# Kernel tuning notes

Measured on AMD Instinct MI355X. Metric: run time of the kernel, lower is better.

## Reference

```python
import jax, jax.numpy as jnp
import numpy as np

NC, NPR, E, B = 200000, 100000, 500000, 200000
DIN, HID, HEADS = 16, 256, 8
D = HID // HEADS
NCOLOR, NSIZE, NGROUP = 1000, 30, 50


def setup_inputs() -> dict:
    key = jax.random.key(0)
    ks = jax.random.split(key, 24)
    g = lambda i, shape, s=0.05: jax.random.normal(ks[i], shape, jnp.float32) * s
    return dict(
        customer_x=g(0, (NC, DIN), 1.0),
        product_x=g(1, (NPR, DIN), 1.0),
        proj_cust_W=g(2, (DIN, HID)), proj_cust_b=jnp.zeros((HID,), jnp.float32),
        proj_prod_W=g(3, (DIN, HID)), proj_prod_b=jnp.zeros((HID,), jnp.float32),
        att_src_r=g(4, (HEADS, D)), att_dst_r=g(5, (HEADS, D)),
        att_src_rb=g(6, (HEADS, D)), att_dst_rb=g(7, (HEADS, D)),
        q_sem=g(8, (HID,)), k_lin_W=g(9, (HID, HID)), k_lin_b=jnp.zeros((HID,), jnp.float32),
        color_emb=g(10, (NCOLOR, 8), 1.0),
        size_emb=g(11, (NSIZE, 4), 1.0),
        group_emb=g(12, (NGROUP, 4), 1.0),
        fc1_W=g(13, (HID * 2 + 16, 128)), fc1_b=jnp.zeros((128,), jnp.float32),
        fc2_W=g(14, (128, 32)), fc2_b=jnp.zeros((32,), jnp.float32),
        fc3_W=g(15, (32, 1)), fc3_b=jnp.zeros((1,), jnp.float32),
        bn1_gamma=jnp.ones((128,), jnp.float32), bn1_beta=jnp.zeros((128,), jnp.float32),
        bn2_gamma=jnp.ones((32,), jnp.float32), bn2_beta=jnp.zeros((32,), jnp.float32),
        edge_src=jax.random.randint(ks[16], (E,), 0, NC),
        edge_dst=jax.random.randint(ks[17], (E,), 0, NPR),
        label_src=jax.random.randint(ks[18], (B,), 0, NC),
        label_dst=jax.random.randint(ks[19], (B,), 0, NPR),
        size_idx=jax.random.randint(ks[20], (B,), 0, NSIZE),
        color_idx=jax.random.randint(ks[21], (B,), 0, NCOLOR),
        group_idx=jax.random.randint(ks[22], (B,), 0, NGROUP),
    )


def _edge_softmax(logits, dst, n):
    # destination-grouped softmax over edges; logits: [E,H]
    m = jax.ops.segment_max(logits, dst, num_segments=n)
    m = jnp.where(jnp.isfinite(m), m, 0.0)
    e = jnp.exp(logits - m[dst])
    s = jax.ops.segment_sum(e, dst, num_segments=n)
    return e / (s[dst] + 1e-16)


def _han_relation(h_src, h_dst, a_src, a_dst, src, dst, n_dst):
    # h_*: [N,H,D]; a_*: [H,D]
    logits = (h_src * a_src).sum(-1)[src] + (h_dst * a_dst).sum(-1)[dst]  # [E,H]
    logits = jax.nn.leaky_relu(logits, 0.2)
    alpha = _edge_softmax(logits, dst, n_dst)
    msg = alpha[:, :, None] * h_src[src]  # [E,H,D]
    out = jax.ops.segment_sum(msg, dst, num_segments=n_dst)
    return jax.nn.relu(out.reshape(n_dst, -1))  # [N_dst, H*D]


def _group(outs, q, kW, kb):
    # semantic attention over metapaths (PyG HANConv group)
    stk = jnp.stack(outs)  # [M,N,F]
    score = (q * jnp.tanh(stk @ kW + kb).mean(1)).sum(-1)  # [M]
    attn = jax.nn.softmax(score)
    return jnp.einsum('m,mnf->nf', attn, stk)


def _bn(x, gamma, beta):
    mu = x.mean(0)
    var = x.var(0)
    return (x - mu) * jax.lax.rsqrt(var + 1e-5) * gamma + beta


def reference(customer_x, product_x, proj_cust_W, proj_cust_b, proj_prod_W, proj_prod_b,
              att_src_r, att_dst_r, att_src_rb, att_dst_rb, q_sem, k_lin_W, k_lin_b,
              color_emb, size_emb, group_emb, fc1_W, fc1_b, fc2_W, fc2_b, fc3_W, fc3_b,
              bn1_gamma, bn1_beta, bn2_gamma, bn2_beta,
              edge_src, edge_dst, label_src, label_dst, size_idx, color_idx, group_idx):
    h_c = (customer_x @ proj_cust_W + proj_cust_b).reshape(-1, HEADS, D)
    h_p = (product_x @ proj_prod_W + proj_prod_b).reshape(-1, HEADS, D)
    # relation customer -returns-> product
    out_p = _han_relation(h_c, h_p, att_src_r, att_dst_r, edge_src, edge_dst, NPR)
    # relation product -returned_by-> customer (reversed edges)
    out_c = _han_relation(h_p, h_c, att_src_rb, att_dst_rb, edge_dst, edge_src, NC)
    cust = _group([out_c], q_sem, k_lin_W, k_lin_b)  # [NC, 256]
    prod = _group([out_p], q_sem, k_lin_W, k_lin_b)  # [NPR, 256]
    feat = jnp.concatenate([cust[label_src], prod[label_dst],
                            size_emb[size_idx], color_emb[color_idx], group_emb[group_idx]], axis=-1)
    x = jax.nn.relu(feat @ fc1_W + fc1_b)
    x = _bn(x, bn1_gamma, bn1_beta)
    x = jax.nn.relu(x @ fc2_W + fc2_b)
    x = _bn(x, bn2_gamma, bn2_beta)
    return x @ fc3_W + fc3_b
```

## Files before the change

kernel.cpp:

```cpp
#include <hip/hip_runtime.h>

#define NCC 200000
#define NPRR 100000
#define NEE 500000
#define NBB 200000

typedef __attribute__((ext_vector_type(8))) short bf16x8;
typedef __attribute__((ext_vector_type(16))) float f32x16;

__device__ __forceinline__ float b2f(unsigned short u){ return __uint_as_float(((unsigned)u)<<16); }
__device__ __forceinline__ unsigned short f2b(float f){
  unsigned x = __float_as_uint(f);
  return (unsigned short)((x + 0x7fffu + ((x>>16)&1u)) >> 16);
}

__global__ __launch_bounds__(256) void wa_prep2(
    const float* __restrict__ Wc, const float* __restrict__ bc,
    const float* __restrict__ attAc, const float* __restrict__ attBc,
    const float* __restrict__ Wp, const float* __restrict__ bp,
    const float* __restrict__ attAp, const float* __restrict__ attBp,
    float* __restrict__ WAc, float* __restrict__ WAp)
{
  int tid = threadIdx.x;
  for (int task = tid; task < 4*17*8; task += 256) {
    int grp = task / 136, rem = task % 136;
    int k = rem >> 3, h = rem & 7;
    const float* att = (grp==0)?attAc:(grp==1)?attBc:(grp==2)?attAp:attBp;
    const float* W   = (grp<2)?Wc:Wp;
    const float* bias= (grp<2)?bc:bp;
    const float* row = (k < 16) ? (W + k*256) : bias;
    float acc = 0.f;
    for (int d = 0; d < 32; d++) acc = fmaf(row[h*32+d], att[h*32+d], acc);
    if (grp<2) WAc[(grp&1)*136 + rem] = acc;
    else       WAp[(grp&1)*136 + rem] = acc;
  }
}

__global__ __launch_bounds__(256) void prep_proj(
    const float* __restrict__ Wc, const float* __restrict__ Wp,
    const float* __restrict__ WAc, const float* __restrict__ WAp,
    unsigned short* __restrict__ WtC, unsigned short* __restrict__ WtP,
    unsigned short* __restrict__ WAtC, unsigned short* __restrict__ WAtP)
{
  int idx = blockIdx.x*256 + threadIdx.x;
  if (idx < 4096){ int n=idx>>4, k=idx&15; WtC[idx]=f2b(Wc[k*256+n]); }
  else if (idx < 8192){ int t=idx-4096; int n=t>>4, k=t&15; WtP[t]=f2b(Wp[k*256+n]); }
  else if (idx < 8704){ int t=idx-8192; int n=t>>4, k=t&15;
    WAtC[t] = (n<16)? f2b(WAc[(n>>3)*136 + k*8 + (n&7)]) : (unsigned short)0; }
  else if (idx < 9216){ int t=idx-8704; int n=t>>4, k=t&15;
    WAtP[t] = (n<16)? f2b(WAp[(n>>3)*136 + k*8 + (n&7)]) : (unsigned short)0; }
}

__global__ __launch_bounds__(256) void prep_fc1(const float* __restrict__ fc1W,
    const float* __restrict__ fc1b,
    const float* __restrict__ size_emb, const float* __restrict__ color_emb,
    const float* __restrict__ group_emb,
    unsigned short* __restrict__ BtC, unsigned short* __restrict__ BtP,
    float* __restrict__ Ts, float* __restrict__ Tc, float* __restrict__ Tg)
{
  int idx = blockIdx.x*256 + threadIdx.x;
  if (idx < 32768){
    int n = idx>>8, k = idx&255;
    BtC[idx] = f2b(fc1W[k*128 + n]);
  } else if (idx < 65536){
    int t = idx - 32768;
    int n = t>>8, k = t&255;
    BtP[t] = f2b(fc1W[(256+k)*128 + n]);
  } else if (idx < 65536 + 30*128){
    int t = idx - 65536;
    int s = t>>7, j = t&127;
    float a = fc1b[j];
    #pragma unroll
    for (int c=0;c<4;c++) a = fmaf(size_emb[s*4+c], fc1W[(512+c)*128+j], a);
    Ts[t] = a;
  } else if (idx < 65536 + 30*128 + 1000*128){
    int t = idx - 65536 - 30*128;
    int col = t>>7, j = t&127;
    float a = 0.f;
    #pragma unroll
    for (int c=0;c<8;c++) a = fmaf(color_emb[col*8+c], fc1W[(516+c)*128+j], a);
    Tc[t] = a;
  } else if (idx < 65536 + 30*128 + 1000*128 + 50*128){
    int t = idx - 65536 - 30*128 - 1000*128;
    int g = t>>7, j = t&127;
    float a = 0.f;
    #pragma unroll
    for (int c=0;c<4;c++) a = fmaf(group_emb[g*4+c], fc1W[(524+c)*128+j], a);
    Tg[t] = a;
  }
}

__global__ __launch_bounds__(256) void proj_mfma(const float* __restrict__ X,
    const unsigned short* __restrict__ Wt, const unsigned short* __restrict__ WAt,
    const float* __restrict__ WA,
    unsigned short* __restrict__ H, float* __restrict__ sA, float* __restrict__ sB,
    int N, int nt)
{
  __shared__ unsigned short wt[4608];
  __shared__ float biasS[16];
  int tid = threadIdx.x;
  for (int i=tid; i<512; i+=256) ((uint4*)wt)[i] = ((const uint4*)Wt)[i];
  for (int i=tid; i<64;  i+=256) ((uint4*)(wt+4096))[i] = ((const uint4*)WAt)[i];
  if (tid < 16) biasS[tid] = WA[(tid>>3)*136 + 128 + (tid&7)];
  __syncthreads();
  int wv = tid>>6, lane = tid&63, m = lane&31, hi = lane>>5;
  for (int t = blockIdx.x; t < nt; t += gridDim.x){
    int node = t*32 + m;
    bf16x8 a;
    {
      const float4* xr = (const float4*)(X + (long long)node*16 + hi*8);
      float4 f0 = xr[0], f1 = xr[1];
      unsigned short av[8] = {f2b(f0.x),f2b(f0.y),f2b(f0.z),f2b(f0.w),
                              f2b(f1.x),f2b(f1.y),f2b(f1.z),f2b(f1.w)};
      a = *(bf16x8*)av;
    }
    #pragma unroll
    for (int s=0;s<2;s++){
      int c0 = wv*64 + s*32;
      bf16x8 b = *(const bf16x8*)(wt + (c0+m)*16 + hi*8);
      f32x16 acc;
      #pragma unroll
      for (int i=0;i<16;i++) acc[i]=0.f;
      acc = __builtin_amdgcn_mfma_f32_32x32x16_bf16(a, b, acc, 0, 0, 0);
      #pragma unroll
      for (int reg=0; reg<16; reg++){
        int row = (reg&3) + 8*(reg>>2) + 4*hi;
        H[(long long)(t*32+row)*256 + c0 + m] = f2b(acc[reg]);
      }
    }
    if (wv == 0){
      bf16x8 b = *(const bf16x8*)(wt + 4096 + m*16 + hi*8);
      f32x16 acc;
      #pragma unroll
      for (int i=0;i<16;i++) acc[i]=0.f;
      acc = __builtin_amdgcn_mfma_f32_32x32x16_bf16(a, b, acc, 0, 0, 0);
      if (m < 16){
        float bias = biasS[m];
        float* dst = (m < 8) ? sA : sB;
        int h = m & 7;
        #pragma unroll
        for (int reg=0; reg<16; reg++){
          int row = (reg&3) + 8*(reg>>2) + 4*hi;
          dst[(long long)(t*32+row)*8 + h] = acc[reg] + bias;
        }
      }
    }
  }
}

__global__ __launch_bounds__(256) void hist2(const int* __restrict__ src, const int* __restrict__ dst,
    int* __restrict__ cnt_c, int* __restrict__ cnt_p, int E)
{
  int e = blockIdx.x*256 + threadIdx.x;
  if (e >= E) return;
  atomicAdd(&cnt_p[dst[e]], 1);
  atomicAdd(&cnt_c[src[e]], 1);
}

__global__ __launch_bounds__(256) void scan_phase1(const int* __restrict__ cnt, int* __restrict__ bsum, int N)
{
  __shared__ int red[256];
  int tid = threadIdx.x;
  int base = blockIdx.x*1024 + tid*4;
  int s = 0;
  #pragma unroll
  for (int k=0;k<4;k++){ int i=base+k; if (i<N) s += cnt[i]; }
  red[tid] = s;
  __syncthreads();
  for (int off=128; off>0; off>>=1){ if (tid<off) red[tid]+=red[tid+off]; __syncthreads(); }
  if (tid==0) bsum[blockIdx.x] = red[0];
}

__global__ __launch_bounds__(256) void scan_phase2(int* __restrict__ bsum, int B,
    int* __restrict__ rowptr, int N)
{
  __shared__ int ts[256];
  int tid = threadIdx.x;
  int v = (tid<B) ? bsum[tid] : 0;
  ts[tid] = v;
  __syncthreads();
  for (int off=1; off<256; off<<=1){
    int t = (tid>=off) ? ts[tid-off] : 0;
    __syncthreads();
    ts[tid] += t;
    __syncthreads();
  }
  if (tid < B) bsum[tid] = ts[tid] - v;
  if (tid == B-1) rowptr[N] = ts[tid];
}

__global__ __launch_bounds__(256) void scan_phase3(const int* __restrict__ cnt,
    const int* __restrict__ bsum, int* __restrict__ rowptr, int N)
{
  __shared__ int ts[256];
  int tid = threadIdx.x;
  int base = blockIdx.x*1024 + tid*4;
  int v[4]; int s = 0;
  #pragma unroll
  for (int k=0;k<4;k++){ int i=base+k; v[k] = (i<N) ? cnt[i] : 0; s += v[k]; }
  ts[tid] = s;
  __syncthreads();
  for (int off=1; off<256; off<<=1){
    int t = (tid>=off) ? ts[tid-off] : 0;
    __syncthreads();
    ts[tid] += t;
    __syncthreads();
  }
  int run = bsum[blockIdx.x] + ts[tid] - s;
  #pragma unroll
  for (int k=0;k<4;k++){ int i=base+k; if (i<N){ rowptr[i]=run; run += v[k]; } }
}

__global__ __launch_bounds__(256) void place2(const int* __restrict__ src, const int* __restrict__ dst,
    const int* __restrict__ rp_r, const int* __restrict__ rp_rb,
    int* __restrict__ cnt_p, int* __restrict__ cnt_c,
    int* __restrict__ si_r, int* __restrict__ si_rb, int E)
{
  int e = blockIdx.x*256 + threadIdx.x;
  if (e >= E) return;
  int s = src[e], d = dst[e];
  si_r [rp_r [d] + atomicAdd(&cnt_p[d], 1)] = s;
  si_rb[rp_rb[s] + atomicAdd(&cnt_c[s], 1)] = d;
}

__global__ __launch_bounds__(256) void agg_gemm(
    const int* __restrict__ rowptr, const int* __restrict__ srcidx,
    const float* __restrict__ sSrc, const float* __restrict__ sDst,
    const unsigned short* __restrict__ H, const unsigned short* __restrict__ Bt,
    unsigned short* __restrict__ Y)
{
  __shared__ unsigned short feat[32*264];
  int tid = threadIdx.x;
  int wv = tid>>6, lane = tid&63;
  int g = lane>>4, ln = lane&15, h = ln>>1;
  long long base = (long long)blockIdx.x*32;
  #pragma unroll
  for (int t=0;t<2;t++){
    int r = wv*8 + t*4 + g;
    long long n = base + r;
    int e  = rowptr[n], e1 = rowptr[n+1];
    float sdh = sDst[n*8 + h];
    float acc[16];
    #pragma unroll
    for (int c=0;c<16;c++) acc[c]=0.f;
    float den = 0.f;
    while (__any(e < e1)){
      if (e < e1){
        int s0 = srcidx[e];
        bool has2 = (e+1 < e1);
        int s1 = has2 ? srcidx[e+1] : s0;
        const uint4* p0 = (const uint4*)&H[(long long)s0*256 + ln*16];
        const uint4* p1 = (const uint4*)&H[(long long)s1*256 + ln*16];
        uint4 uA0 = p0[0], uA1 = p0[1];
        uint4 uB0 = p1[0], uB1 = p1[1];
        float l0 = sSrc[(long long)s0*8 + h] + sdh;
        float l1 = sSrc[(long long)s1*8 + h] + sdh;
        float w0 = __expf(l0 > 0.f ? l0 : 0.2f*l0);
        float w1 = has2 ? __expf(l1 > 0.f ? l1 : 0.2f*l1) : 0.f;
        den += w0 + w1;
        unsigned ua[8] = {uA0.x,uA0.y,uA0.z,uA0.w, uA1.x,uA1.y,uA1.z,uA1.w};
        unsigned ub[8] = {uB0.x,uB0.y,uB0.z,uB0.w, uB1.x,uB1.y,uB1.z,uB1.w};
        #pragma unroll
        for (int p=0;p<8;p++){
          acc[p*2]   = fmaf(w0, b2f((unsigned short)(ua[p]&0xffffu)), acc[p*2]);
          acc[p*2+1] = fmaf(w0, b2f((unsigned short)(ua[p]>>16)),     acc[p*2+1]);
          acc[p*2]   = fmaf(w1, b2f((unsigned short)(ub[p]&0xffffu)), acc[p*2]);
          acc[p*2+1] = fmaf(w1, b2f((unsigned short)(ub[p]>>16)),     acc[p*2+1]);
        }
        e += 2;
      }
    }
    float inv = 1.f/(den + 1e-16f);
    unsigned short ov[16];
    #pragma unroll
    for (int c=0;c<16;c++) ov[c] = f2b(fmaxf(acc[c]*inv, 0.f));
    *(uint4*)&feat[r*264 + ln*16]     = *(uint4*)&ov[0];
    *(uint4*)&feat[r*264 + ln*16 + 8] = *(uint4*)&ov[8];
  }
  __syncthreads();
  int m = lane&31, hi = lane>>5;
  f32x16 acc;
  #pragma unroll
  for (int i=0;i<16;i++) acc[i]=0.f;
  const unsigned short* ap  = feat + m*264 + hi*8;
  const unsigned short* btp = Bt + (wv*32 + m)*256 + hi*8;
  #pragma unroll 4
  for (int ks=0; ks<16; ks++){
    bf16x8 a = *(const bf16x8*)(ap + ks*16);
    bf16x8 b = *(const bf16x8*)(btp + ks*16);
    acc = __builtin_amdgcn_mfma_f32_32x32x16_bf16(a, b, acc, 0, 0, 0);
  }
  int col = wv*32 + m;
  #pragma unroll
  for (int reg=0; reg<16; reg++){
    int row = (reg&3) + 8*(reg>>2) + 4*hi;
    Y[(base+row)*128 + col] = f2b(acc[reg]);
  }
}

__global__ __launch_bounds__(256) void gather_fc1(
    const unsigned short* __restrict__ Yc, const unsigned short* __restrict__ Yp,
    const float* __restrict__ Ts, const float* __restrict__ Tc, const float* __restrict__ Tg,
    const int* __restrict__ lsrc, const int* __restrict__ ldst,
    const int* __restrict__ sidx, const int* __restrict__ cidx, const int* __restrict__ gidx,
    unsigned short* __restrict__ x1, float* __restrict__ bnsum, int ntiles)
{
  __shared__ float redS[16][128];
  __shared__ float redQ[16][128];
  int tid = threadIdx.x;
  int rl = tid>>4, g = tid&15;
  float sacc[8] = {0,0,0,0,0,0,0,0};
  float qacc[8] = {0,0,0,0,0,0,0,0};
  for (int t = blockIdx.x; t < ntiles; t += gridDim.x){
    long long row = (long long)t*16 + rl;
    int ls = lsrc[row], ld = ldst[row], si = sidx[row], ci = cidx[row], gi = gidx[row];
    uint4 uc = *(const uint4*)&Yc[(long long)ls*128 + g*8];
    uint4 up = *(const uint4*)&Yp[(long long)ld*128 + g*8];
    float4 t0 = *(const float4*)&Ts[si*128 + g*8];
    float4 t1 = *(const float4*)&Ts[si*128 + g*8 + 4];
    float4 c0 = *(const float4*)&Tc[ci*128 + g*8];
    float4 c1 = *(const float4*)&Tc[ci*128 + g*8 + 4];
    float4 g0 = *(const float4*)&Tg[gi*128 + g*8];
    float4 g1 = *(const float4*)&Tg[gi*128 + g*8 + 4];
    unsigned ucs[4] = {uc.x,uc.y,uc.z,uc.w};
    unsigned ups[4] = {up.x,up.y,up.z,up.w};
    float tb[8] = {t0.x+c0.x+g0.x, t0.y+c0.y+g0.y, t0.z+c0.z+g0.z, t0.w+c0.w+g0.w,
                   t1.x+c1.x+g1.x, t1.y+c1.y+g1.y, t1.z+c1.z+g1.z, t1.w+c1.w+g1.w};
    unsigned short ov[8];
    #pragma unroll
    for (int p=0;p<4;p++){
      float vl = b2f((unsigned short)(ucs[p]&0xffffu)) + b2f((unsigned short)(ups[p]&0xffffu)) + tb[p*2];
      float vh = b2f((unsigned short)(ucs[p]>>16))     + b2f((unsigned short)(ups[p]>>16))     + tb[p*2+1];
      vl = fmaxf(vl, 0.f); vh = fmaxf(vh, 0.f);
      ov[p*2] = f2b(vl); ov[p*2+1] = f2b(vh);
      sacc[p*2]   += vl; qacc[p*2]   += vl*vl;
      sacc[p*2+1] += vh; qacc[p*2+1] += vh*vh;
    }
    *(uint4*)&x1[row*128 + g*8] = *(uint4*)ov;
  }
  #pragma unroll
  for (int j=0;j<8;j++){ redS[rl][g*8+j]=sacc[j]; redQ[rl][g*8+j]=qacc[j]; }
  __syncthreads();
  if (tid < 128){
    float s=0.f, q=0.f;
    #pragma unroll
    for (int r=0;r<16;r++){ s += redS[r][tid]; q += redQ[r][tid]; }
    atomicAdd(&bnsum[tid], s);
    atomicAdd(&bnsum[128+tid], q);
  }
}

__global__ void bn1_fold(const float* __restrict__ bnsum,
    const float* __restrict__ gamma, const float* __restrict__ beta,
    const float* __restrict__ fc2W, const float* __restrict__ fc2b,
    unsigned short* __restrict__ Bt2, float* __restrict__ b2p, float invB)
{
  __shared__ float sc[128], sh[128];
  int tid = threadIdx.x;
  if (tid<128){
    float mu  = bnsum[tid]*invB;
    float var = bnsum[128+tid]*invB - mu*mu;
    float s = gamma[tid] * rsqrtf(var + 1e-5f);
    sc[tid]=s; sh[tid]= beta[tid] - mu*s;
  }
  __syncthreads();
  for (int idx=tid; idx<32*128; idx+=256){
    int n = idx>>7, k = idx&127;
    Bt2[idx] = f2b(sc[k]*fc2W[k*32+n]);
  }
  if (tid<32){
    float a = fc2b[tid];
    for (int k=0;k<128;k++) a = fmaf(sh[k], fc2W[k*32+tid], a);
    b2p[tid]=a;
  }
}

__global__ __launch_bounds__(256) void fc2_mfma(const unsigned short* __restrict__ x1,
    const unsigned short* __restrict__ Bt2, const float* __restrict__ b2p,
    unsigned short* __restrict__ x2, float* __restrict__ bnsum2, int M)
{
  __shared__ unsigned short xt[128*136];
  __shared__ unsigned short wt[32*136];
  __shared__ float redS[4][32];
  __shared__ float redQ[4][32];
  int tid = threadIdx.x;
  long long base = (long long)blockIdx.x*128;
  for (int idx=tid; idx<128*16; idx+=256){
    int r = idx>>4, c = idx&15;
    uint4 u = make_uint4(0,0,0,0);
    if (base + r < M) u = *(const uint4*)&x1[(base+r)*128 + c*8];
    *(uint4*)&xt[r*136 + c*8] = u;
  }
  for (int idx=tid; idx<32*16; idx+=256){
    int r = idx>>4, c = idx&15;
    *(uint4*)&wt[r*136 + c*8] = *(const uint4*)&Bt2[r*128 + c*8];
  }
  __syncthreads();
  int wv = tid>>6, lane = tid&63;
  int m = lane&31, hi = lane>>5;
  f32x16 acc;
  #pragma unroll
  for (int i=0;i<16;i++) acc[i]=0.f;
  const unsigned short* ap = xt + (wv*32 + m)*136 + hi*8;
  const unsigned short* bp = wt + m*136 + hi*8;
  #pragma unroll
  for (int ks=0; ks<8; ks++){
    bf16x8 a = *(const bf16x8*)(ap + ks*16);
    bf16x8 b = *(const bf16x8*)(bp + ks*16);
    acc = __builtin_amdgcn_mfma_f32_32x32x16_bf16(a, b, acc, 0, 0, 0);
  }
  int col = m;
  float bias = b2p[col];
  float s=0.f, q=0.f;
  #pragma unroll
  for (int reg=0; reg<16; reg++){
    int row = (reg&3) + 8*(reg>>2) + 4*hi;
    long long grow = base + wv*32 + row;
    float v = fmaxf(acc[reg] + bias, 0.f);
    if (grow < M) x2[grow*32 + col] = f2b(v);
    s += v; q += v*v;
  }
  if (base + 128 > M){
    s = 0.f; q = 0.f;
    #pragma unroll
    for (int reg=0; reg<16; reg++){
      int row = (reg&3) + 8*(reg>>2) + 4*hi;
      long long grow = base + wv*32 + row;
      float v = fmaxf(acc[reg] + bias, 0.f);
      if (grow < M){ s += v; q += v*v; }
    }
  }
  s += __shfl_xor(s, 32);
  q += __shfl_xor(q, 32);
  if (hi == 0){ redS[wv][col] = s; redQ[wv][col] = q; }
  __syncthreads();
  if (tid < 32){
    float a = redS[0][tid]+redS[1][tid]+redS[2][tid]+redS[3][tid];
    float b = redQ[0][tid]+redQ[1][tid]+redQ[2][tid]+redQ[3][tid];
    atomicAdd(&bnsum2[tid], a);
    atomicAdd(&bnsum2[32+tid], b);
  }
}

__global__ void bn2_fold(const float* __restrict__ bnsum2,
    const float* __restrict__ gamma2, const float* __restrict__ beta2,
    const float* __restrict__ fc3W, const float* __restrict__ fc3b,
    float* __restrict__ w3p, float invB)
{
  __shared__ float sh3[32];
  int tid = threadIdx.x;
  if (tid<32){
    float mu  = bnsum2[tid]*invB;
    float var = bnsum2[32+tid]*invB - mu*mu;
    float s   = gamma2[tid] * rsqrtf(var + 1e-5f);
    float shv = beta2[tid] - mu*s;
    float w   = fc3W[tid];
    w3p[tid]  = s*w;
    sh3[tid]  = shv*w;
  }
  __syncthreads();
  if (tid==0){
    float a = fc3b[0];
    for (int j=0;j<32;j++) a += sh3[j];
    w3p[32] = a;
  }
}

__global__ __launch_bounds__(256) void fc3_kernel(const unsigned short* __restrict__ x2,
    const float* __restrict__ w3p, float* __restrict__ out)
{
  __shared__ float wl[34];
  int tid = threadIdx.x;
  if (tid<33) wl[tid]=w3p[tid];
  __syncthreads();
  long long row = (long long)blockIdx.x*32 + (tid>>3);
  int j0 = (tid&7)*4;
  uint2 u = *(const uint2*)(x2 + row*32 + j0);
  float a = b2f((unsigned short)(u.x&0xffffu))*wl[j0]
          + b2f((unsigned short)(u.x>>16))   *wl[j0+1]
          + b2f((unsigned short)(u.y&0xffffu))*wl[j0+2]
          + b2f((unsigned short)(u.y>>16))   *wl[j0+3];
  a += __shfl_xor(a,1);
  a += __shfl_xor(a,2);
  a += __shfl_xor(a,4);
  if ((tid&7)==0) out[row] = a + wl[32];
}

extern "C" void kernel_launch(void* const* d_in, const int* in_sizes, int n_in,
                              void* d_out, int out_size, void* d_ws, size_t ws_size,
                              hipStream_t stream)
{
  (void)in_sizes; (void)n_in; (void)out_size; (void)ws_size;
  const float* customer_x = (const float*)d_in[0];
  const float* product_x  = (const float*)d_in[1];
  const float* pcW = (const float*)d_in[2];
  const float* pcB = (const float*)d_in[3];
  const float* ppW = (const float*)d_in[4];
  const float* ppB = (const float*)d_in[5];
  const float* att_src_r  = (const float*)d_in[6];
  const float* att_dst_r  = (const float*)d_in[7];
  const float* att_src_rb = (const float*)d_in[8];
  const float* att_dst_rb = (const float*)d_in[9];
  const float* color_emb = (const float*)d_in[13];
  const float* size_emb  = (const float*)d_in[14];
  const float* group_emb = (const float*)d_in[15];
  const float* fc1W = (const float*)d_in[16];
  const float* fc1b = (const float*)d_in[17];
  const float* fc2W = (const float*)d_in[18];
  const float* fc2b = (const float*)d_in[19];
  const float* fc3W = (const float*)d_in[20];
  const float* fc3b = (const float*)d_in[21];
  const float* bn1g = (const float*)d_in[22];
  const float* bn1b = (const float*)d_in[23];
  const float* bn2g = (const float*)d_in[24];
  const float* bn2b = (const float*)d_in[25];
  const int* edge_src  = (const int*)d_in[26];
  const int* edge_dst  = (const int*)d_in[27];
  const int* label_src = (const int*)d_in[28];
  const int* label_dst = (const int*)d_in[29];
  const int* size_idx  = (const int*)d_in[30];
  const int* color_idx = (const int*)d_in[31];
  const int* group_idx = (const int*)d_in[32];

  char* ws = (char*)d_ws;
  size_t off = 0;
  auto alloc = [&](size_t bytes)->char* {
    char* p = ws + off;
    off += (bytes + 255) & ~(size_t)255;
    return p;
  };
  unsigned short* H_c  = (unsigned short*)alloc((size_t)NCC*256*2);
  unsigned short* H_p  = (unsigned short*)alloc((size_t)NPRR*256*2);
  unsigned short* slab = (unsigned short*)alloc((size_t)NPRR*256*2);
  float* s_cr     = (float*)alloc((size_t)NCC*8*4);
  float* s_crb    = (float*)alloc((size_t)NCC*8*4);
  float* s_pr     = (float*)alloc((size_t)NPRR*8*4);
  float* s_prb    = (float*)alloc((size_t)NPRR*8*4);
  int* rowptr_r   = (int*)alloc((size_t)(NPRR+1)*4);
  int* rowptr_rb  = (int*)alloc((size_t)(NCC+1)*4);
  int* srcidx_r   = (int*)alloc((size_t)NEE*4);
  int* srcidx_rb  = (int*)alloc((size_t)NEE*4);
  int* cnts       = (int*)alloc((size_t)(NCC+NPRR)*2*4);
  int* cnt_c      = cnts;
  int* cnt_p      = cnts + NCC;
  int* cnt_c2     = cnts + NCC + NPRR;
  int* cnt_p2     = cnts + NCC + NPRR + NCC;
  int* bsum_c     = (int*)alloc(256*4);
  int* bsum_p     = (int*)alloc(256*4);
  unsigned short* BtC = (unsigned short*)alloc(128*256*2);
  unsigned short* BtP = (unsigned short*)alloc(128*256*2);
  float* Ts     = (float*)alloc(30*128*4);
  float* Tc     = (float*)alloc(1000*128*4);
  float* Tg     = (float*)alloc(50*128*4);
  float* wa_c   = (float*)alloc(272*4);
  float* wa_p   = (float*)alloc(272*4);
  unsigned short* WtC  = (unsigned short*)alloc(256*16*2);
  unsigned short* WtP  = (unsigned short*)alloc(256*16*2);
  unsigned short* WAtC = (unsigned short*)alloc(32*16*2);
  unsigned short* WAtP = (unsigned short*)alloc(32*16*2);
  float* bnsum1 = (float*)alloc(256*4);
  float* bnsum2 = (float*)alloc(64*4);
  unsigned short* Bt2 = (unsigned short*)alloc(32*128*2);
  float* b2p    = (float*)alloc(32*4);
  float* w3p    = (float*)alloc(34*4);
  unsigned short* Y_p = slab;
  unsigned short* Y_c = H_c;
  unsigned short* x1b = H_p;
  unsigned short* x2b = (unsigned short*)s_cr;

  hipMemsetAsync(bnsum1, 0, 1280, stream);
  hipMemsetAsync(cnts, 0, (size_t)(NCC+NPRR)*2*4, stream);

  wa_prep2<<<1,256,0,stream>>>(pcW, pcB, att_src_r, att_dst_rb,
                               ppW, ppB, att_dst_r, att_src_rb, wa_c, wa_p);
  prep_proj<<<36,256,0,stream>>>(pcW, ppW, wa_c, wa_p, WtC, WtP, WAtC, WAtP);
  prep_fc1<<<(203776+255)/256,256,0,stream>>>(fc1W, fc1b, size_emb, color_emb, group_emb,
      BtC, BtP, Ts, Tc, Tg);

  proj_mfma<<<2048,256,0,stream>>>(customer_x, WtC, WAtC, wa_c, H_c, s_cr, s_crb, NCC, NCC/32);
  proj_mfma<<<2048,256,0,stream>>>(product_x,  WtP, WAtP, wa_p, H_p, s_pr, s_prb, NPRR, NPRR/32);

  const int eg = (NEE+255)/256;
  const int BP = (NPRR+1023)/1024;
  const int BC = (NCC +1023)/1024;
  hist2<<<eg,256,0,stream>>>(edge_src, edge_dst, cnt_c, cnt_p, NEE);
  scan_phase1<<<BP,256,0,stream>>>(cnt_p, bsum_p, NPRR);
  scan_phase2<<<1,256,0,stream>>>(bsum_p, BP, rowptr_r, NPRR);
  scan_phase3<<<BP,256,0,stream>>>(cnt_p, bsum_p, rowptr_r, NPRR);
  scan_phase1<<<BC,256,0,stream>>>(cnt_c, bsum_c, NCC);
  scan_phase2<<<1,256,0,stream>>>(bsum_c, BC, rowptr_rb, NCC);
  scan_phase3<<<BC,256,0,stream>>>(cnt_c, bsum_c, rowptr_rb, NCC);
  place2<<<eg,256,0,stream>>>(edge_src, edge_dst, rowptr_r, rowptr_rb,
      cnt_p2, cnt_c2, srcidx_r, srcidx_rb, NEE);

  agg_gemm<<<NPRR/32,256,0,stream>>>(rowptr_r,  srcidx_r,  s_cr,  s_pr,  H_c, BtP, Y_p);
  agg_gemm<<<NCC/32,256,0,stream>>>(rowptr_rb, srcidx_rb, s_prb, s_crb, H_p, BtC, Y_c);

  gather_fc1<<<2048,256,0,stream>>>(Y_c, Y_p, Ts, Tc, Tg,
      label_src, label_dst, size_idx, color_idx, group_idx, x1b, bnsum1, NBB/16);

  bn1_fold<<<1,256,0,stream>>>(bnsum1, bn1g, bn1b, fc2W, fc2b, Bt2, b2p, 1.0f/NBB);
  fc2_mfma<<<(NBB+127)/128,256,0,stream>>>(x1b, Bt2, b2p, x2b, bnsum2, NBB);
  bn2_fold<<<1,64,0,stream>>>(bnsum2, bn2g, bn2b, fc3W, fc3b, w3p, 1.0f/NBB);
  fc3_kernel<<<NBB/32,256,0,stream>>>(x2b, w3p, (float*)d_out);
}
```

Measured before the change: 591.2 us.

## Stage edge-chunk gathers into double-buffered LDS with async global_load_lds in agg_gemm

The aggregation in agg_gemm is restructured so the whole block walks its contiguous edge range in chunks of 64 edges. For each chunk, the gathered source rows of H and the source attention scores are copied into LDS with `__builtin_amdgcn_global_load_lds`, double-buffered with explicit vmcnt waits and barriers. Each 16-lane group then accumulates two destination rows from LDS instead of issuing its own scattered global loads. This is meant to overlap gather latency with compute and balance memory traffic across the block. In exchange it uses about 68 KB of LDS per block, which lowers occupancy, adds two barriers per chunk, and makes each group walk its rows serially.

```diff
diff --git a/kernel.cpp b/kernel.cpp
--- a/kernel.cpp
+++ b/kernel.cpp
@@ -7,6 +7,9 @@
 
 typedef __attribute__((ext_vector_type(8))) short bf16x8;
 typedef __attribute__((ext_vector_type(16))) float f32x16;
+
+typedef __attribute__((address_space(1))) const void gvoid_t;
+typedef __attribute__((address_space(3))) void lvoid_t;
 
 __device__ __forceinline__ float b2f(unsigned short u){ return __uint_as_float(((unsigned)u)<<16); }
 __device__ __forceinline__ unsigned short f2b(float f){
@@ -223,78 +226,135 @@
   si_rb[rp_rb[s] + atomicAdd(&cnt_c[s], 1)] = d;
 }
 
+#define CH 64
 __global__ __launch_bounds__(256) void agg_gemm(
     const int* __restrict__ rowptr, const int* __restrict__ srcidx,
     const float* __restrict__ sSrc, const float* __restrict__ sDst,
     const unsigned short* __restrict__ H, const unsigned short* __restrict__ Bt,
     unsigned short* __restrict__ Y)
 {
-  __shared__ unsigned short feat[32*264];
+  __shared__ __align__(1024) char smem[69632];
+  unsigned short* feat = (unsigned short*)smem;
   int tid = threadIdx.x;
   int wv = tid>>6, lane = tid&63;
-  int g = lane>>4, ln = lane&15, h = ln>>1;
   long long base = (long long)blockIdx.x*32;
-  #pragma unroll
-  for (int t=0;t<2;t++){
-    int r = wv*8 + t*4 + g;
-    long long n = base + r;
-    int e  = rowptr[n], e1 = rowptr[n+1];
-    float sdh = sDst[n*8 + h];
-    float acc[16];
-    #pragma unroll
-    for (int c=0;c<16;c++) acc[c]=0.f;
-    float den = 0.f;
-    while (__any(e < e1)){
-      if (e < e1){
-        int s0 = srcidx[e];
-        bool has2 = (e+1 < e1);
-        int s1 = has2 ? srcidx[e+1] : s0;
-        const uint4* p0 = (const uint4*)&H[(long long)s0*256 + ln*16];
-        const uint4* p1 = (const uint4*)&H[(long long)s1*256 + ln*16];
-        uint4 uA0 = p0[0], uA1 = p0[1];
-        uint4 uB0 = p1[0], uB1 = p1[1];
-        float l0 = sSrc[(long long)s0*8 + h] + sdh;
-        float l1 = sSrc[(long long)s1*8 + h] + sdh;
-        float w0 = __expf(l0 > 0.f ? l0 : 0.2f*l0);
-        float w1 = has2 ? __expf(l1 > 0.f ? l1 : 0.2f*l1) : 0.f;
-        den += w0 + w1;
-        unsigned ua[8] = {uA0.x,uA0.y,uA0.z,uA0.w, uA1.x,uA1.y,uA1.z,uA1.w};
-        unsigned ub[8] = {uB0.x,uB0.y,uB0.z,uB0.w, uB1.x,uB1.y,uB1.z,uB1.w};
-        #pragma unroll
-        for (int p=0;p<8;p++){
-          acc[p*2]   = fmaf(w0, b2f((unsigned short)(ua[p]&0xffffu)), acc[p*2]);
-          acc[p*2+1] = fmaf(w0, b2f((unsigned short)(ua[p]>>16)),     acc[p*2+1]);
-          acc[p*2]   = fmaf(w1, b2f((unsigned short)(ub[p]&0xffffu)), acc[p*2]);
-          acc[p*2+1] = fmaf(w1, b2f((unsigned short)(ub[p]>>16)),     acc[p*2+1]);
+  int E0 = rowptr[base], E1 = rowptr[base+32];
+  int K = E1 - E0;
+  int nc = (K + CH - 1) / CH;
+  int gi = tid>>4, ln = tid&15, h = ln>>1;
+  long long n0 = base + gi*2;
+  int e0a = rowptr[n0], e1a = rowptr[n0+1], e1b = rowptr[n0+2];
+  float sdh0 = sDst[n0*8 + h];
+  float sdh1 = sDst[(n0+1)*8 + h];
+  float acc0[16], acc1[16];
+  #pragma unroll
+  for (int i=0;i<16;i++){ acc0[i]=0.f; acc1[i]=0.f; }
+  float den0 = 0.f, den1 = 0.f;
+
+  auto STAGE = [&](int c, int b){
+    int cbase = E0 + c*CH;
+    int elast = E1 - 1;
+    #pragma unroll
+    for (int i=0;i<8;i++){
+      int rl = wv*16 + 2*i + (lane>>5);
+      int sv = srcidx[min(cbase + rl, elast)];
+      const unsigned short* gp = H + (long long)sv*256 + (lane&31)*8;
+      char* lp = smem + b*32768 + (wv*16 + 2*i)*512;
+      __builtin_amdgcn_global_load_lds((gvoid_t*)gp, (lvoid_t*)lp, 16, 0, 0);
+    }
+    #pragma unroll
+    for (int j=0;j<2;j++){
+      int el = wv*16 + j*8 + (lane>>3);
+      int sv = srcidx[min(cbase + el, elast)];
+      const float* gp = sSrc + (long long)sv*8 + (lane&7);
+      char* lp = smem + 65536 + b*2048 + (wv*16 + j*8)*32;
+      __builtin_amdgcn_global_load_lds((gvoid_t*)gp, (lvoid_t*)lp, 4, 0, 0);
+    }
+  };
+
+  if (nc > 0){
+    STAGE(0, 0);
+    asm volatile("s_waitcnt vmcnt(0)" ::: "memory");
+    __builtin_amdgcn_s_barrier();
+    for (int c = 0; c < nc; ++c){
+      int b = c & 1;
+      if (c + 1 < nc){
+        STAGE(c+1, b^1);
+        asm volatile("s_waitcnt vmcnt(10)" ::: "memory");
+      } else {
+        asm volatile("s_waitcnt vmcnt(0)" ::: "memory");
+      }
+      __builtin_amdgcn_s_barrier();
+      int off = E0 + c*CH;
+      const unsigned short* sb = (const unsigned short*)(smem + b*32768);
+      const float* sc = (const float*)(smem + 65536 + b*2048);
+      {
+        int lo = max(e0a - off, 0), hi = min(e1a - off, CH);
+        for (int r = lo; r < hi; ++r){
+          float lv = sc[r*8 + h] + sdh0;
+          float w = __expf(lv > 0.f ? lv : 0.2f*lv);
+          den0 += w;
+          uint4 u0 = *(const uint4*)(sb + r*256 + ln*16);
+          uint4 u1 = *(const uint4*)(sb + r*256 + ln*16 + 8);
+          unsigned uu[8] = {u0.x,u0.y,u0.z,u0.w, u1.x,u1.y,u1.z,u1.w};
+          #pragma unroll
+          for (int p=0;p<8;p++){
+            acc0[p*2]   = fmaf(w, b2f((unsigned short)(uu[p]&0xffffu)), acc0[p*2]);
+            acc0[p*2+1] = fmaf(w, b2f((unsigned short)(uu[p]>>16)),     acc0[p*2+1]);
+          }
         }
-        e += 2;
       }
-    }
-    float inv = 1.f/(den + 1e-16f);
+      {
+        int lo = max(e1a - off, 0), hi = min(e1b - off, CH);
+        for (int r = lo; r < hi; ++r){
+          float lv = sc[r*8 + h] + sdh1;
+          float w = __expf(lv > 0.f ? lv : 0.2f*lv);
+          den1 += w;
+          uint4 u0 = *(const uint4*)(sb + r*256 + ln*16);
+          uint4 u1 = *(const uint4*)(sb + r*256 + ln*16 + 8);
+          unsigned uu[8] = {u0.x,u0.y,u0.z,u0.w, u1.x,u1.y,u1.z,u1.w};
+          #pragma unroll
+          for (int p=0;p<8;p++){
+            acc1[p*2]   = fmaf(w, b2f((unsigned short)(uu[p]&0xffffu)), acc1[p*2]);
+            acc1[p*2+1] = fmaf(w, b2f((unsigned short)(uu[p]>>16)),     acc1[p*2+1]);
+          }
+        }
+      }
+      __builtin_amdgcn_s_barrier();
+    }
+  }
+
+  {
+    float inv0 = 1.f/(den0 + 1e-16f);
     unsigned short ov[16];
     #pragma unroll
-    for (int c=0;c<16;c++) ov[c] = f2b(fmaxf(acc[c]*inv, 0.f));
-    *(uint4*)&feat[r*264 + ln*16]     = *(uint4*)&ov[0];
-    *(uint4*)&feat[r*264 + ln*16 + 8] = *(uint4*)&ov[8];
+    for (int c2=0;c2<16;c2++) ov[c2] = f2b(fmaxf(acc0[c2]*inv0, 0.f));
+    *(uint4*)&feat[(gi*2)*264 + ln*16]     = *(uint4*)&ov[0];
+    *(uint4*)&feat[(gi*2)*264 + ln*16 + 8] = *(uint4*)&ov[8];
+    float inv1 = 1.f/(den1 + 1e-16f);
+    #pragma unroll
+    for (int c2=0;c2<16;c2++) ov[c2] = f2b(fmaxf(acc1[c2]*inv1, 0.f));
+    *(uint4*)&feat[(gi*2+1)*264 + ln*16]     = *(uint4*)&ov[0];
+    *(uint4*)&feat[(gi*2+1)*264 + ln*16 + 8] = *(uint4*)&ov[8];
   }
   __syncthreads();
   int m = lane&31, hi = lane>>5;
-  f32x16 acc;
-  #pragma unroll
-  for (int i=0;i<16;i++) acc[i]=0.f;
+  f32x16 accm;
+  #pragma unroll
+  for (int i=0;i<16;i++) accm[i]=0.f;
   const unsigned short* ap  = feat + m*264 + hi*8;
   const unsigned short* btp = Bt + (wv*32 + m)*256 + hi*8;
   #pragma unroll 4
   for (int ks=0; ks<16; ks++){
     bf16x8 a = *(const bf16x8*)(ap + ks*16);
     bf16x8 b = *(const bf16x8*)(btp + ks*16);
-    acc = __builtin_amdgcn_mfma_f32_32x32x16_bf16(a, b, acc, 0, 0, 0);
+    accm = __builtin_amdgcn_mfma_f32_32x32x16_bf16(a, b, accm, 0, 0, 0);
   }
   int col = wv*32 + m;
   #pragma unroll
   for (int reg=0; reg<16; reg++){
     int row = (reg&3) + 8*(reg>>2) + 4*hi;
-    Y[(base+row)*128 + col] = f2b(acc[reg]);
+    Y[(base+row)*128 + col] = f2b(accm[reg]);
   }
 }
 
```

New measurement: 627.8 us. 6.2% more time.
